# Optimization experiments

Measured on AMD Instinct MI355X. Metric: run time of the kernel, lower is better.

Reference implementation:

```python
import jax, jax.numpy as jnp
import numpy as np

B, N, C = 2, 4096, 256
H = 8          # num heads
D = C // H     # head dim = 32
SR = 2         # spatial reduction ratio
HID = 1024     # mixffn hidden = 4*C
EPS = 1e-5


def layernorm(x, g, b):
    mu = jnp.mean(x, axis=-1, keepdims=True)
    var = jnp.mean(jnp.square(x - mu), axis=-1, keepdims=True)
    return (x - mu) * jax.lax.rsqrt(var + EPS) * g + b


def conv2d(x, w, b, stride, pad, groups=1):
    out = jax.lax.conv_general_dilated(
        x, w, (stride, stride), [(pad, pad), (pad, pad)],
        dimension_numbers=("NCHW", "OIHW", "NCHW"), feature_group_count=groups)
    return out + b[None, :, None, None]


def setup_inputs() -> dict:
    key = jax.random.key(0)
    ks = jax.random.split(key, 20)
    s = lambda k, shape, scale=0.02: jax.random.normal(k, shape, jnp.float32) * scale
    return {
        "x": jax.random.normal(ks[0], (B, N, C), jnp.float32),
        "h": 64, "w": 64,
        "ln1_g": jnp.ones((C,), jnp.float32), "ln1_b": jnp.zeros((C,), jnp.float32),
        "q_w": s(ks[1], (C, C)),
        "kv_w": s(ks[2], (2 * C, C)),
        "sr_w": s(ks[3], (C, C, SR, SR)), "sr_b": jnp.zeros((C,), jnp.float32),
        "srn_g": jnp.ones((C,), jnp.float32), "srn_b": jnp.zeros((C,), jnp.float32),
        "proj_w": s(ks[4], (C, C)), "proj_b": jnp.zeros((C,), jnp.float32),
        "ln2_g": jnp.ones((C,), jnp.float32), "ln2_b": jnp.zeros((C,), jnp.float32),
        "fc1_w": s(ks[5], (HID, C)), "fc1_b": jnp.zeros((HID,), jnp.float32),
        "pe_w": s(ks[6], (HID, 1, 3, 3)), "pe_b": jnp.zeros((HID,), jnp.float32),
        "fc2_w": s(ks[7], (C, HID)), "fc2_b": jnp.zeros((C,), jnp.float32),
    }


def reference(x, h, w, ln1_g, ln1_b, q_w, kv_w, sr_w, sr_b, srn_g, srn_b,
              proj_w, proj_b, ln2_g, ln2_b, fc1_w, fc1_b, pe_w, pe_b, fc2_w, fc2_b):
    b_, n_, c_ = x.shape
    # ---- attention branch ----
    xn = layernorm(x, ln1_g, ln1_b)
    q = jnp.einsum("bnc,oc->bno", xn, q_w).reshape(b_, n_, H, D).transpose(0, 2, 1, 3)  # [B,H,N,D]
    # spatial-reduction of KV
    x_kv = xn.reshape(b_, h, w, c_).transpose(0, 3, 1, 2)              # [B,C,h,w]
    x_kv = conv2d(x_kv, sr_w, sr_b, stride=SR, pad=0)                  # [B,C,h/SR,w/SR]
    nkv = (h // SR) * (w // SR)
    x_kv = x_kv.reshape(b_, c_, nkv).transpose(0, 2, 1)                # [B,Nkv,C]
    x_kv = layernorm(x_kv, srn_g, srn_b)
    kv = jnp.einsum("bnc,oc->bno", x_kv, kv_w).reshape(b_, nkv, 2, H, D)
    k = kv[:, :, 0].transpose(0, 2, 1, 3)                              # [B,H,Nkv,D]
    v = kv[:, :, 1].transpose(0, 2, 1, 3)
    scale = D ** -0.5
    att = jax.nn.softmax(jnp.einsum("bhxd,bhyd->bhxy", q, k) * scale, axis=-1)
    o = jnp.einsum("bhxy,bhyd->bhxd", att, v)                          # [B,H,N,D]
    o = o.transpose(0, 2, 1, 3).reshape(b_, n_, c_)
    o = jnp.einsum("bnc,oc->bno", o, proj_w) + proj_b
    x = x + o
    # ---- Mix-FFN branch ----
    xn2 = layernorm(x, ln2_g, ln2_b)
    xf = xn2.reshape(b_, h, w, c_).transpose(0, 3, 1, 2)               # [B,C,h,w]
    xf = jnp.einsum("bchw,oc->bohw", xf, fc1_w) + fc1_b[None, :, None, None]
    xf = conv2d(xf, pe_w, pe_b, stride=1, pad=1, groups=HID)           # depthwise 3x3
    xf = jax.nn.gelu(xf, approximate=False)
    xf = jnp.einsum("bchw,oc->bohw", xf, fc2_w) + fc2_b[None, :, None, None]
    xf = xf.transpose(0, 2, 3, 1).reshape(b_, n_, c_)
    return x + xf
```

## Files before the change

### kernel.cpp

```cpp
#include <hip/hip_runtime.h>
#include <math.h>

constexpr int BB   = 2;
constexpr int NN   = 4096;
constexpr int CCH  = 256;
constexpr int NH   = 8;
constexpr int HD   = 32;
constexpr int GW   = 64;
constexpr int NKV  = 1024;
constexpr int HIDN = 1024;
constexpr float EPSF = 1e-5f;

typedef short  bf16x8 __attribute__((ext_vector_type(8)));
typedef short  bf16x4 __attribute__((ext_vector_type(4)));
typedef float  f32x4  __attribute__((ext_vector_type(4)));

__device__ __forceinline__ short f2bf(float f) {
    unsigned int u = __float_as_uint(f);
    unsigned int r = (u + 0x7FFFu + ((u >> 16) & 1u)) >> 16;
    return (short)r;
}
__device__ __forceinline__ float bf2f(short s) {
    return __uint_as_float(((unsigned int)(unsigned short)s) << 16);
}
__device__ __forceinline__ void gl16(const void* g, void* l) {
    __builtin_amdgcn_global_load_lds(
        (const __attribute__((address_space(1))) void*)g,
        (__attribute__((address_space(3))) void*)l, 16, 0, 0);
}

__global__ __launch_bounds__(256) void prep_kernel(const float* __restrict__ q_w,
                                                   const float* __restrict__ kv_w,
                                                   const float* __restrict__ proj_w,
                                                   const float* __restrict__ fc1_w,
                                                   const float* __restrict__ fc2_w,
                                                   const float* __restrict__ sr_w,
                                                   short* qwb, short* kvwb, short* pjwb,
                                                   short* f1wb, short* f2wb, short* srwb,
                                                   const float* __restrict__ x,
                                                   const float* __restrict__ ln1_g,
                                                   const float* __restrict__ ln1_b,
                                                   short* __restrict__ xn) {
    __shared__ float pa[4], pb[4];
    int t = threadIdx.x;
    if (blockIdx.x < 4096) {
        int i = blockIdx.x * 256 + t;
        if (i < 65536) { qwb[i] = f2bf(q_w[i] * 0.17677669529663687f); return; }
        i -= 65536;
        if (i < 131072) { kvwb[i] = f2bf(kv_w[i]); return; }
        i -= 131072;
        if (i < 65536) { pjwb[i] = f2bf(proj_w[i]); return; }
        i -= 65536;
        if (i < 262144) { f1wb[i] = f2bf(fc1_w[i]); return; }
        i -= 262144;
        if (i < 262144) { f2wb[i] = f2bf(fc2_w[i]); return; }
        i -= 262144;
        {
            int o = i >> 10, rem = i & 1023, c = rem >> 2, q = rem & 3;
            srwb[o * 1024 + q * 256 + c] = f2bf(sr_w[i]);
        }
        return;
    }
    int row = blockIdx.x - 4096;
    float v = x[row * CCH + t];
    float a = v, b = v * v;
#pragma unroll
    for (int off = 32; off > 0; off >>= 1) {
        a += __shfl_xor(a, off);
        b += __shfl_xor(b, off);
    }
    int w = t >> 6;
    if ((t & 63) == 0) { pa[w] = a; pb[w] = b; }
    __syncthreads();
    a = pa[0] + pa[1] + pa[2] + pa[3];
    b = pb[0] + pb[1] + pb[2] + pb[3];
    float mu = a * (1.0f / CCH);
    float var = b * (1.0f / CCH) - mu * mu;
    float rs = rsqrtf(var + EPSF);
    xn[row * CCH + t] = f2bf((v - mu) * rs * ln1_g[t] + ln1_b[t]);
}

template <bool INBF>
__global__ __launch_bounds__(256) void ln_wave(const void* __restrict__ in,
                                               const float* __restrict__ g,
                                               const float* __restrict__ bta,
                                               short* __restrict__ out) {
    int t = threadIdx.x;
    int w = t >> 6, lane = t & 63;
    int row = blockIdx.x * 4 + w;
    float v[4];
    if (INBF) {
        bf16x4 bv = *(const bf16x4*)&((const short*)in)[(size_t)row * CCH + lane * 4];
#pragma unroll
        for (int j = 0; j < 4; j++) v[j] = bf2f(bv[j]);
    } else {
        float4 fv = *(const float4*)&((const float*)in)[(size_t)row * CCH + lane * 4];
        v[0] = fv.x; v[1] = fv.y; v[2] = fv.z; v[3] = fv.w;
    }
    float a = v[0] + v[1] + v[2] + v[3];
    float b = v[0]*v[0] + v[1]*v[1] + v[2]*v[2] + v[3]*v[3];
#pragma unroll
    for (int off = 1; off < 64; off <<= 1) {
        a += __shfl_xor(a, off);
        b += __shfl_xor(b, off);
    }
    float mu = a * (1.0f / CCH);
    float var = b * (1.0f / CCH) - mu * mu;
    float rs = rsqrtf(var + EPSF);
    bf16x4 ov;
#pragma unroll
    for (int j = 0; j < 4; j++)
        ov[j] = f2bf((v[j] - mu) * rs * g[lane * 4 + j] + bta[lane * 4 + j]);
    *(bf16x4*)&out[(size_t)row * CCH + lane * 4] = ov;
}

template <bool OUTB, int RESMODE>
__device__ __forceinline__ void gemm64_body(const short* __restrict__ A,
                                            const short* __restrict__ W,
                                            const float* __restrict__ bias,
                                            const void* __restrict__ res,
                                            void* __restrict__ outp,
                                            int M, int O, int K, int bx, int by,
                                            short (*As0)[64], short (*Ws0)[64],
                                            short (*As1)[64], short (*Ws1)[64]) {
    int t = threadIdx.x;
    int m0 = by * 64, o0 = bx * 64;
    int w = t >> 6, lane = t & 63;
    int wm = (w >> 1) * 32, wn = (w & 1) * 32;
    int fr = lane & 15, fq = lane >> 4;
    int srow = lane >> 3;
    int sg   = (lane & 7) ^ srow;
    f32x4 acc[2][2];
#pragma unroll
    for (int mi = 0; mi < 2; mi++)
#pragma unroll
        for (int ni = 0; ni < 2; ni++)
            acc[mi][ni] = f32x4{0.f, 0.f, 0.f, 0.f};

    auto stage = [&](short (*Asb)[64], short (*Wsb)[64], int k0) {
#pragma unroll
        for (int r = 0; r < 2; r++) {
            int rowA = r * 32 + w * 8 + srow;
            gl16(&A[(size_t)(m0 + rowA) * K + k0 + sg * 8], &Asb[r * 32 + w * 8][0]);
            gl16(&W[(size_t)(o0 + rowA) * K + k0 + sg * 8], &Wsb[r * 32 + w * 8][0]);
        }
    };
    auto compute = [&](short (*Asb)[64], short (*Wsb)[64]) {
#pragma unroll
        for (int half = 0; half < 2; half++) {
            bf16x8 af[2], wf[2];
#pragma unroll
            for (int mi = 0; mi < 2; mi++) {
                int row = wm + mi * 16 + fr;
                af[mi] = *(const bf16x8*)&Asb[row][(((half << 2) | fq) ^ (row & 7)) * 8];
            }
#pragma unroll
            for (int ni = 0; ni < 2; ni++) {
                int row = wn + ni * 16 + fr;
                wf[ni] = *(const bf16x8*)&Wsb[row][(((half << 2) | fq) ^ (row & 7)) * 8];
            }
#pragma unroll
            for (int mi = 0; mi < 2; mi++)
#pragma unroll
                for (int ni = 0; ni < 2; ni++)
                    acc[mi][ni] = __builtin_amdgcn_mfma_f32_16x16x32_bf16(
                        af[mi], wf[ni], acc[mi][ni], 0, 0, 0);
        }
    };

    stage(As0, Ws0, 0);
    __syncthreads();
    for (int k0 = 0; k0 < K; k0 += 128) {
        if (k0 + 64 < K) stage(As1, Ws1, k0 + 64);
        compute(As0, Ws0);
        __syncthreads();
        if (k0 + 128 < K) stage(As0, Ws0, k0 + 128);
        if (k0 + 64 < K) compute(As1, Ws1);
        __syncthreads();
    }
#pragma unroll
    for (int mi = 0; mi < 2; mi++)
#pragma unroll
        for (int ni = 0; ni < 2; ni++)
#pragma unroll
            for (int r = 0; r < 4; r++) {
                int m = m0 + wm + mi * 16 + fq * 4 + r;
                int o = o0 + wn + ni * 16 + fr;
                float v = acc[mi][ni][r];
                if (bias) v += bias[o];
                if (RESMODE == 1) v += ((const float*)res)[(size_t)m * O + o];
                if (RESMODE == 2) v += bf2f(((const short*)res)[(size_t)m * O + o]);
                if (OUTB) ((short*)outp)[(size_t)m * O + o] = f2bf(v);
                else      ((float*)outp)[(size_t)m * O + o] = v;
            }
}

template <bool OUTB, int RESMODE>
__global__ __launch_bounds__(256, 4) void gemm64(const short* __restrict__ A,
                                                 const short* __restrict__ W,
                                                 const float* __restrict__ bias,
                                                 const void* __restrict__ res,
                                                 void* __restrict__ outp,
                                                 int M, int O, int K) {
    __shared__ short As0[64][64], Ws0[64][64];
    __shared__ short As1[64][64], Ws1[64][64];
    gemm64_body<OUTB, RESMODE>(A, W, bias, res, outp, M, O, K,
                               blockIdx.x, blockIdx.y, As0, Ws0, As1, Ws1);
}

__device__ __forceinline__ void sr_body(const short* __restrict__ xn,
                                        const short* __restrict__ Wsr,
                                        const float* __restrict__ sr_b,
                                        float* __restrict__ srtmp, int bx, int by,
                                        short (*As0)[64], short (*As1)[64],
                                        short (*Ws0)[64], short (*Ws1)[64]) {
    int t = threadIdx.x;
    int m0 = by * 32, o0 = bx * 64;
    int w = t >> 6, lane = t & 63;
    int wm = (w >> 1) * 16, wn = (w & 1) * 32;
    int fr = lane & 15, fq = lane >> 4;
    int srow = lane >> 3;
    int sg   = (lane & 7) ^ srow;
    int arow = w * 8 + srow;
    int p = m0 + arow;
    int b = p >> 10, pp = p & 1023, ii = pp >> 5, jj = pp & 31;
    int nbase = ii * 128 + jj * 2;
    size_t xbase = (size_t)(b * NN) * CCH;
    f32x4 acc[2];
    acc[0] = f32x4{0.f, 0.f, 0.f, 0.f};
    acc[1] = f32x4{0.f, 0.f, 0.f, 0.f};

    auto stage = [&](short (*Asb)[64], short (*Wsb)[64], int k0) {
        int q = k0 >> 8, c0 = k0 & 255;
        int n = nbase + (q >> 1) * 64 + (q & 1);
        gl16(&xn[xbase + (size_t)n * CCH + c0 + sg * 8], &Asb[w * 8][0]);
#pragma unroll
        for (int r = 0; r < 2; r++)
            gl16(&Wsr[(size_t)(o0 + r * 32 + w * 8 + srow) * 1024 + k0 + sg * 8],
                 &Wsb[r * 32 + w * 8][0]);
    };
    auto compute = [&](short (*Asb)[64], short (*Wsb)[64]) {
#pragma unroll
        for (int half = 0; half < 2; half++) {
            int cg = (half << 2) | fq;
            int rowa = wm + fr;
            bf16x8 af = *(const bf16x8*)&Asb[rowa][(cg ^ (rowa & 7)) * 8];
            bf16x8 wf[2];
#pragma unroll
            for (int ni = 0; ni < 2; ni++) {
                int row = wn + ni * 16 + fr;
                wf[ni] = *(const bf16x8*)&Wsb[row][(cg ^ (row & 7)) * 8];
            }
#pragma unroll
            for (int ni = 0; ni < 2; ni++)
                acc[ni] = __builtin_amdgcn_mfma_f32_16x16x32_bf16(
                    af, wf[ni], acc[ni], 0, 0, 0);
        }
    };

    stage(As0, Ws0, 0);
    __syncthreads();
    for (int k0 = 0; k0 < 1024; k0 += 128) {
        if (k0 + 64 < 1024) stage(As1, Ws1, k0 + 64);
        compute(As0, Ws0);
        __syncthreads();
        if (k0 + 128 < 1024) stage(As0, Ws0, k0 + 128);
        compute(As1, Ws1);
        __syncthreads();
    }
#pragma unroll
    for (int ni = 0; ni < 2; ni++)
#pragma unroll
        for (int r = 0; r < 4; r++) {
            int m = m0 + wm + fq * 4 + r;
            int o = o0 + wn + ni * 16 + fr;
            srtmp[(size_t)m * CCH + o] = acc[ni][r] + sr_b[o];
        }
}

__global__ __launch_bounds__(256, 4) void qsr_gemm(const short* __restrict__ xn,
                                                   const short* __restrict__ qwb,
                                                   short* __restrict__ qb,
                                                   const short* __restrict__ srwb,
                                                   const float* __restrict__ sr_b,
                                                   float* __restrict__ srtmp) {
    __shared__ short pool[16384];
    int i = blockIdx.x;
    if (i < 512) {
        gemm64_body<true, 0>(xn, qwb, nullptr, nullptr, qb, BB * NN, CCH, CCH,
                             i & 3, i >> 2,
                             (short(*)[64])(pool),
                             (short(*)[64])(pool + 4096),
                             (short(*)[64])(pool + 8192),
                             (short(*)[64])(pool + 12288));
    } else {
        i -= 512;
        sr_body(xn, srwb, sr_b, srtmp, i & 3, i >> 2,
                (short(*)[64])(pool),
                (short(*)[64])(pool + 2048),
                (short(*)[64])(pool + 4096),
                (short(*)[64])(pool + 8192));
    }
}

__global__ __launch_bounds__(256, 2) void gemm_fc1(const short* __restrict__ A,
                                                   const short* __restrict__ W,
                                                   const float* __restrict__ bias,
                                                   short* __restrict__ outp,
                                                   int M, int O, int K) {
    __shared__ short As0[128][64], Ws0[128][64];
    __shared__ short As1[128][64], Ws1[128][64];
    int t = threadIdx.x;
    int m0 = blockIdx.y * 128, o0 = blockIdx.x * 128;
    int w = t >> 6, lane = t & 63;
    int wm = (w >> 1) * 64, wn = (w & 1) * 64;
    int fr = lane & 15, fq = lane >> 4;
    int srow = lane >> 3;
    int sg   = (lane & 7) ^ srow;
    f32x4 acc[4][4];
#pragma unroll
    for (int mi = 0; mi < 4; mi++)
#pragma unroll
        for (int ni = 0; ni < 4; ni++)
            acc[mi][ni] = f32x4{0.f, 0.f, 0.f, 0.f};

    auto stage = [&](short (*Asb)[64], short (*Wsb)[64], int k0) {
#pragma unroll
        for (int r = 0; r < 4; r++) {
            int rowA = r * 32 + w * 8 + srow;
            gl16(&A[(size_t)(m0 + rowA) * K + k0 + sg * 8], &Asb[r * 32 + w * 8][0]);
            gl16(&W[(size_t)(o0 + rowA) * K + k0 + sg * 8], &Wsb[r * 32 + w * 8][0]);
        }
    };
    auto compute = [&](short (*Asb)[64], short (*Wsb)[64]) {
#pragma unroll
        for (int half = 0; half < 2; half++) {
            bf16x8 af[4], wf[4];
#pragma unroll
            for (int mi = 0; mi < 4; mi++) {
                int row = wm + mi * 16 + fr;
                af[mi] = *(const bf16x8*)&Asb[row][(((half << 2) | fq) ^ (row & 7)) * 8];
            }
#pragma unroll
            for (int ni = 0; ni < 4; ni++) {
                int row = wn + ni * 16 + fr;
                wf[ni] = *(const bf16x8*)&Wsb[row][(((half << 2) | fq) ^ (row & 7)) * 8];
            }
#pragma unroll
            for (int mi = 0; mi < 4; mi++)
#pragma unroll
                for (int ni = 0; ni < 4; ni++)
                    acc[mi][ni] = __builtin_amdgcn_mfma_f32_16x16x32_bf16(
                        af[mi], wf[ni], acc[mi][ni], 0, 0, 0);
        }
    };

    stage(As0, Ws0, 0);
    __syncthreads();
    for (int k0 = 0; k0 < K; k0 += 128) {
        if (k0 + 64 < K) stage(As1, Ws1, k0 + 64);
        compute(As0, Ws0);
        __syncthreads();
        if (k0 + 128 < K) stage(As0, Ws0, k0 + 128);
        if (k0 + 64 < K) compute(As1, Ws1);
        __syncthreads();
    }
#pragma unroll
    for (int mi = 0; mi < 4; mi++)
#pragma unroll
        for (int ni = 0; ni < 4; ni++)
#pragma unroll
            for (int r = 0; r < 4; r++) {
                int m = m0 + wm + mi * 16 + fq * 4 + r;
                int o = o0 + wn + ni * 16 + fr;
                outp[(size_t)m * O + o] = f2bf(acc[mi][ni][r] + bias[o]);
            }
}

__global__ __launch_bounds__(256, 4) void kv_gemm(const short* __restrict__ A,
                                                  const short* __restrict__ W,
                                                  short* __restrict__ kvk,
                                                  short* __restrict__ vt) {
    __shared__ short As0[64][64], Ws0[64][64];
    __shared__ short As1[64][64], Ws1[64][64];
    int t = threadIdx.x;
    int m0 = blockIdx.y * 64, o0 = blockIdx.x * 64;
    int w = t >> 6, lane = t & 63;
    int wm = (w >> 1) * 32, wn = (w & 1) * 32;
    int fr = lane & 15, fq = lane >> 4;
    int srow = lane >> 3;
    int sg   = (lane & 7) ^ srow;
    f32x4 acc[2][2];
#pragma unroll
    for (int mi = 0; mi < 2; mi++)
#pragma unroll
        for (int ni = 0; ni < 2; ni++)
            acc[mi][ni] = f32x4{0.f, 0.f, 0.f, 0.f};

    auto stage = [&](short (*Asb)[64], short (*Wsb)[64], int k0) {
#pragma unroll
        for (int r = 0; r < 2; r++) {
            int rowA = r * 32 + w * 8 + srow;
            gl16(&A[(size_t)(m0 + rowA) * CCH + k0 + sg * 8], &Asb[r * 32 + w * 8][0]);
            gl16(&W[(size_t)(o0 + rowA) * CCH + k0 + sg * 8], &Wsb[r * 32 + w * 8][0]);
        }
    };
    auto compute = [&](short (*Asb)[64], short (*Wsb)[64]) {
#pragma unroll
        for (int half = 0; half < 2; half++) {
            bf16x8 af[2], wf[2];
#pragma unroll
            for (int mi = 0; mi < 2; mi++) {
                int row = wm + mi * 16 + fr;
                af[mi] = *(const bf16x8*)&Asb[row][(((half << 2) | fq) ^ (row & 7)) * 8];
            }
#pragma unroll
            for (int ni = 0; ni < 2; ni++) {
                int row = wn + ni * 16 + fr;
                wf[ni] = *(const bf16x8*)&Wsb[row][(((half << 2) | fq) ^ (row & 7)) * 8];
            }
#pragma unroll
            for (int mi = 0; mi < 2; mi++)
#pragma unroll
                for (int ni = 0; ni < 2; ni++)
                    acc[mi][ni] = __builtin_amdgcn_mfma_f32_16x16x32_bf16(
                        af[mi], wf[ni], acc[mi][ni], 0, 0, 0);
        }
    };

    stage(As0, Ws0, 0);
    __syncthreads();
    stage(As1, Ws1, 64);
    compute(As0, Ws0);
    __syncthreads();
    stage(As0, Ws0, 128);
    compute(As1, Ws1);
    __syncthreads();
    stage(As1, Ws1, 192);
    compute(As0, Ws0);
    __syncthreads();
    compute(As1, Ws1);

#pragma unroll
    for (int mi = 0; mi < 2; mi++)
#pragma unroll
        for (int ni = 0; ni < 2; ni++) {
            int o = o0 + wn + ni * 16 + fr;
            int mbase = m0 + wm + mi * 16 + fq * 4;
            if (o < 256) {
#pragma unroll
                for (int r = 0; r < 4; r++)
                    kvk[(size_t)(mbase + r) * 256 + o] = f2bf(acc[mi][ni][r]);
            } else {
                int h = (o - 256) >> 5, d = (o - 256) & 31;
                int b = mbase >> 10, y0 = mbase & 1023;
                bf16x4 pv;
#pragma unroll
                for (int r = 0; r < 4; r++) pv[r] = f2bf(acc[mi][ni][r]);
                *(bf16x4*)&vt[((size_t)((b * NH + h) * HD) + d) * NKV + y0] = pv;
            }
        }
}

__global__ __launch_bounds__(256, 3) void attn_mfma(const short* __restrict__ qb,
                                                    const short* __restrict__ kvk,
                                                    const short* __restrict__ vt,
                                                    short* __restrict__ o) {
    int blk = blockIdx.x;
    int qt = blk & 31; int hh = (blk >> 5) & 7; int b = blk >> 8;
    int t = threadIdx.x; int w = t >> 6; int lane = t & 63;
    int fr = lane & 15, fq = lane >> 4;
    __shared__ short Ks0[128][32], Ks1[128][32];
    __shared__ short Vt0[64][64],  Vt1[64][64];
    __shared__ short Ps[4][2][16][64];
    int n0 = qt * 128 + w * 16;
    bf16x8 qa[2];
#pragma unroll
    for (int mi = 0; mi < 2; mi++)
        qa[mi] = *(const bf16x8*)&qb[((size_t)(b * NN) + n0 + mi * 64 + fr) * CCH + hh * HD + fq * 8];
    f32x4 oacc[2][2];
    float lst[2][4];
#pragma unroll
    for (int mi = 0; mi < 2; mi++) {
#pragma unroll
        for (int nd = 0; nd < 2; nd++) oacc[mi][nd] = f32x4{0.f, 0.f, 0.f, 0.f};
#pragma unroll
        for (int r = 0; r < 4; r++) lst[mi][r] = 0.f;
    }

    int srowK = lane >> 2;
    int sgK   = (lane & 3) ^ (srowK & 3);
    int srowV = lane >> 3;
    int sgV   = (lane & 7) ^ srowV;

    auto stageKV = [&](short (*Ksb)[32], short (*Vtb)[64], int y0) {
#pragma unroll
        for (int r2 = 0; r2 < 2; r2++) {
            int rowK = r2 * 64 + w * 16 + srowK;
            gl16(&kvk[((size_t)(b * NKV) + y0 + rowK) * 256 + hh * HD + sgK * 8],
                 &Ksb[r2 * 64 + w * 16][0]);
        }
#pragma unroll
        for (int r3 = 0; r3 < 2; r3++) {
            int d = w * 8 + srowV;
            gl16(&vt[((size_t)((b * NH + hh) * HD) + d) * NKV + y0 + r3 * 64 + sgV * 8],
                 &Vtb[r3 * 32 + w * 8][0]);
        }
    };
    auto tile = [&](short (*Ksb)[32], short (*Vtb)[64]) {
#pragma unroll
        for (int h2 = 0; h2 < 2; h2++) {
#pragma unroll
            for (int mi = 0; mi < 2; mi++) {
                f32x4 s[4];
#pragma unroll
                for (int ni = 0; ni < 4; ni++) {
                    int rowk = h2 * 64 + ni * 16 + fr;
                    bf16x8 kb = *(const bf16x8*)&Ksb[rowk][(fq ^ (fr & 3)) * 8];
                    s[ni] = __builtin_amdgcn_mfma_f32_16x16x32_bf16(
                        qa[mi], kb, f32x4{0.f, 0.f, 0.f, 0.f}, 0, 0, 0);
                }
#pragma unroll
                for (int r = 0; r < 4; r++) {
                    int row = fq * 4 + r;
                    float psum = 0.f;
#pragma unroll
                    for (int i = 0; i < 4; i++) {
                        float p = __expf(fminf(s[i][r], 30.f));
                        psum += p;
                        int col = i * 16 + fr;
                        int sgp = ((col >> 3) ^ row) & 7;
                        Ps[w][mi][row][sgp * 8 + (col & 7)] = f2bf(p);
                    }
                    lst[mi][r] += psum;
                }
#pragma unroll
                for (int ks = 0; ks < 2; ks++) {
                    int gk = ks * 4 + fq;
                    bf16x8 pa = *(const bf16x8*)&Ps[w][mi][fr][((gk ^ fr) & 7) * 8];
#pragma unroll
                    for (int nd = 0; nd < 2; nd++) {
                        int rowv = nd * 16 + fr;
                        bf16x8 vb = *(const bf16x8*)&Vtb[h2 * 32 + rowv][((gk ^ (rowv & 7)) & 7) * 8];
                        oacc[mi][nd] = __builtin_amdgcn_mfma_f32_16x16x32_bf16(
                            pa, vb, oacc[mi][nd], 0, 0, 0);
                    }
                }
            }
        }
    };

    stageKV(Ks0, Vt0, 0);
    __syncthreads();
    for (int y0 = 0; y0 < NKV; y0 += 256) {
        if (y0 + 128 < NKV) stageKV(Ks1, Vt1, y0 + 128);
        tile(Ks0, Vt0);
        __syncthreads();
        if (y0 + 256 < NKV) stageKV(Ks0, Vt0, y0 + 256);
        tile(Ks1, Vt1);
        __syncthreads();
    }
#pragma unroll
    for (int mi = 0; mi < 2; mi++)
#pragma unroll
        for (int r = 0; r < 4; r++) {
            float ls = lst[mi][r];
#pragma unroll
            for (int off = 1; off < 16; off <<= 1)
                ls += __shfl_xor(ls, off);
            float inv = 1.f / ls;
            int row = n0 + mi * 64 + fq * 4 + r;
#pragma unroll
            for (int nd = 0; nd < 2; nd++)
                o[((size_t)(b * NN) + row) * CCH + hh * HD + nd * 16 + fr] =
                    f2bf(oacc[mi][nd][r] * inv);
        }
}

__global__ __launch_bounds__(256, 2) void dwconv_gelu(const short* __restrict__ xf,
                                                      const float* __restrict__ pe_w,
                                                      const float* __restrict__ pe_b,
                                                      short* __restrict__ out) {
    int blk = blockIdx.x;
    int cg = blk & 15, sp = (blk >> 4) & 15, b = blk >> 8;
    int r0 = (sp >> 2) * 16, c0 = (sp & 3) * 16;
    int ch0 = cg * 64;
    int t = threadIdx.x;
    __shared__ short tile[18][18][64];
    for (int idx = t; idx < 18 * 18 * 8; idx += 256) {
        int pix = idx >> 3, part = idx & 7;
        int row = pix / 18, col = pix - row * 18;
        int gr = r0 + row - 1, gc = c0 + col - 1;
        bf16x8 v = {0, 0, 0, 0, 0, 0, 0, 0};
        if (gr >= 0 && gr < 64 && gc >= 0 && gc < 64)
            v = *(const bf16x8*)&xf[((size_t)(b * NN) + gr * GW + gc) * HIDN + ch0 + part * 8];
        *(bf16x8*)&tile[row][col][part * 8] = v;
    }
    __syncthreads();
    int cl = t & 63, sg = t >> 6;
    int ch = ch0 + cl;
    float wv[9];
#pragma unroll
    for (int k = 0; k < 9; k++) wv[k] = pe_w[ch * 9 + k];
    float bias = pe_b[ch];
#pragma unroll
    for (int q = 0; q < 4; q++) {
        int lr = sg * 4 + q;
        float cA[3], cB[3], cC[3];
#pragma unroll
        for (int ki = 0; ki < 3; ki++) {
            cA[ki] = bf2f(tile[lr + ki][0][cl]);
            cB[ki] = bf2f(tile[lr + ki][1][cl]);
        }
        for (int cc = 0; cc < 16; cc++) {
#pragma unroll
            for (int ki = 0; ki < 3; ki++) cC[ki] = bf2f(tile[lr + ki][cc + 2][cl]);
            float acc = bias;
#pragma unroll
            for (int ki = 0; ki < 3; ki++)
                acc += cA[ki] * wv[ki * 3] + cB[ki] * wv[ki * 3 + 1] + cC[ki] * wv[ki * 3 + 2];
            float z = 0.7978845608f * (acc + 0.044715f * acc * acc * acc);
            float e = __expf(-2.f * fabsf(z));
            float th = (1.f - e) / (1.f + e);
            th = (z < 0.f) ? -th : th;
            float gg = 0.5f * acc * (1.f + th);
            out[((size_t)(b * NN) + (r0 + lr) * GW + c0 + cc) * HIDN + ch] = f2bf(gg);
#pragma unroll
            for (int ki = 0; ki < 3; ki++) { cA[ki] = cB[ki]; cB[ki] = cC[ki]; }
        }
    }
}

extern "C" void kernel_launch(void* const* d_in, const int* in_sizes, int n_in,
                              void* d_out, int out_size, void* d_ws, size_t ws_size,
                              hipStream_t stream) {
    const float* x      = (const float*)d_in[0];
    const float* ln1_g  = (const float*)d_in[3];
    const float* ln1_b  = (const float*)d_in[4];
    const float* q_w    = (const float*)d_in[5];
    const float* kv_w   = (const float*)d_in[6];
    const float* sr_w   = (const float*)d_in[7];
    const float* sr_b   = (const float*)d_in[8];
    const float* srn_g  = (const float*)d_in[9];
    const float* srn_b  = (const float*)d_in[10];
    const float* proj_w = (const float*)d_in[11];
    const float* proj_b = (const float*)d_in[12];
    const float* ln2_g  = (const float*)d_in[13];
    const float* ln2_b  = (const float*)d_in[14];
    const float* fc1_w  = (const float*)d_in[15];
    const float* fc1_b  = (const float*)d_in[16];
    const float* pe_w   = (const float*)d_in[17];
    const float* pe_b   = (const float*)d_in[18];
    const float* fc2_w  = (const float*)d_in[19];
    const float* fc2_b  = (const float*)d_in[20];
    float* out = (float*)d_out;

    char* base = (char*)d_ws;
    short* xn    = (short*)(base);
    short* qb    = (short*)(base + (4ull  << 20));
    float* srtmp = (float*)(base + (12ull << 20));
    short* xkvn  = (short*)(base + (14ull << 20));
    short* kvk   = (short*)(base + (15ull << 20));
    short* vtb   = (short*)(base + (17ull << 20));
    short* obf   = (short*)(base + (18ull << 20));
    short* x1    = (short*)(base + (22ull << 20));
    short* xf1   = (short*)(base + (30ull << 20));
    short* xf2g  = (short*)(base + (46ull << 20));
    short* qwb   = (short*)(base + (62ull << 20));
    short* kvwb  = qwb  + 65536;
    short* pjwb  = kvwb + 131072;
    short* f1wb  = pjwb + 65536;
    short* f2wb  = f1wb + 262144;
    short* srwb  = f2wb + 262144;

    prep_kernel<<<4096 + BB * NN, 256, 0, stream>>>(q_w, kv_w, proj_w, fc1_w, fc2_w, sr_w,
                                                    qwb, kvwb, pjwb, f1wb, f2wb, srwb,
                                                    x, ln1_g, ln1_b, xn);
    qsr_gemm<<<768, 256, 0, stream>>>(xn, qwb, qb, srwb, sr_b, srtmp);
    ln_wave<false><<<BB * NKV / 4, 256, 0, stream>>>(srtmp, srn_g, srn_b, xkvn);
    {
        dim3 g(512 / 64, (BB * NKV) / 64);
        kv_gemm<<<g, 256, 0, stream>>>(xkvn, kvwb, kvk, vtb);
    }
    attn_mfma<<<BB * NH * (NN / 128), 256, 0, stream>>>(qb, kvk, vtb, obf);
    {
        dim3 g(CCH / 64, (BB * NN) / 64);
        gemm64<true, 1><<<g, 256, 0, stream>>>(obf, pjwb, proj_b, x, x1, BB * NN, CCH, CCH);
    }
    ln_wave<true><<<BB * NN / 4, 256, 0, stream>>>(x1, ln2_g, ln2_b, xn);
    {
        dim3 g(HIDN / 128, (BB * NN) / 128);
        gemm_fc1<<<g, 256, 0, stream>>>(xn, f1wb, fc1_b, xf1, BB * NN, HIDN, CCH);
    }
    dwconv_gelu<<<BB * 256, 256, 0, stream>>>(xf1, pe_w, pe_b, xf2g);
    {
        dim3 g(CCH / 64, (BB * NN) / 64);
        gemm64<false, 2><<<g, 256, 0, stream>>>(xf2g, f2wb, fc2_b, x1, out, BB * NN, CCH, HIDN);
    }
}
```

Baseline: 116.7 us.

## Permute key order in V^T and P to pack bf16 conversion and vector LDS stores

The KV projection epilogue now writes V^T with key indices permuted inside each 64-key block. This lets the attention kernel give each lane four contiguous P columns, convert them with v_cvt_pk_bf16_f32 and store them as a single 8-byte LDS write instead of four scalar 2-byte stores. It also adds s_setprio around the MFMA sections to favour matrix issue across waves. The cost is that the V^T writes become scattered scalar stores in the projection epilogue.

After: 115.6 us, median of 2. Within noise of the previous version (-0.9%).

```diff
diff --git a/kernel.cpp b/kernel.cpp
--- a/kernel.cpp
+++ b/kernel.cpp
@@ -22,6 +22,11 @@
 }
 __device__ __forceinline__ float bf2f(short s) {
     return __uint_as_float(((unsigned int)(unsigned short)s) << 16);
+}
+__device__ __forceinline__ unsigned int cvtpk_bf16(float a, float b) {
+    unsigned int r;
+    asm("v_cvt_pk_bf16_f32 %0, %1, %2" : "=v"(r) : "v"(a), "v"(b));
+    return r;
 }
 __device__ __forceinline__ void gl16(const void* g, void* l) {
     __builtin_amdgcn_global_load_lds(
@@ -454,10 +459,14 @@
             } else {
                 int h = (o - 256) >> 5, d = (o - 256) & 31;
                 int b = mbase >> 10, y0 = mbase & 1023;
-                bf16x4 pv;
-#pragma unroll
-                for (int r = 0; r < 4; r++) pv[r] = f2bf(acc[mi][ni][r]);
-                *(bf16x4*)&vt[((size_t)((b * NH + h) * HD) + d) * NKV + y0] = pv;
+                size_t rowbase = ((size_t)((b * NH + h) * HD) + d) * NKV + (y0 >> 6) * 64;
+                int y4 = y0 & 63;
+#pragma unroll
+                for (int r = 0; r < 4; r++) {
+                    int y64 = y4 + r;
+                    int s = (y64 & 15) * 4 + (y64 >> 4);
+                    vt[rowbase + s] = f2bf(acc[mi][ni][r]);
+                }
             }
         }
 }
@@ -513,6 +522,7 @@
 #pragma unroll
             for (int mi = 0; mi < 2; mi++) {
                 f32x4 s[4];
+                __builtin_amdgcn_s_setprio(1);
 #pragma unroll
                 for (int ni = 0; ni < 4; ni++) {
                     int rowk = h2 * 64 + ni * 16 + fr;
@@ -520,32 +530,34 @@
                     s[ni] = __builtin_amdgcn_mfma_f32_16x16x32_bf16(
                         qa[mi], kb, f32x4{0.f, 0.f, 0.f, 0.f}, 0, 0, 0);
                 }
+                __builtin_amdgcn_s_setprio(0);
 #pragma unroll
                 for (int r = 0; r < 4; r++) {
                     int row = fq * 4 + r;
-                    float psum = 0.f;
-#pragma unroll
-                    for (int i = 0; i < 4; i++) {
-                        float p = __expf(fminf(s[i][r], 30.f));
-                        psum += p;
-                        int col = i * 16 + fr;
-                        int sgp = ((col >> 3) ^ row) & 7;
-                        Ps[w][mi][row][sgp * 8 + (col & 7)] = f2bf(p);
-                    }
-                    lst[mi][r] += psum;
+                    float p0 = __expf(fminf(s[0][r], 30.f));
+                    float p1 = __expf(fminf(s[1][r], 30.f));
+                    float p2 = __expf(fminf(s[2][r], 30.f));
+                    float p3 = __expf(fminf(s[3][r], 30.f));
+                    lst[mi][r] += (p0 + p1) + (p2 + p3);
+                    unsigned int w0 = cvtpk_bf16(p0, p1);
+                    unsigned int w1 = cvtpk_bf16(p2, p3);
+                    int gp = (fr >> 1) ^ (row & 7);
+                    *(uint2*)&Ps[w][mi][row][gp * 8 + (fr & 1) * 4] = make_uint2(w0, w1);
                 }
+                __builtin_amdgcn_s_setprio(1);
 #pragma unroll
                 for (int ks = 0; ks < 2; ks++) {
                     int gk = ks * 4 + fq;
-                    bf16x8 pa = *(const bf16x8*)&Ps[w][mi][fr][((gk ^ fr) & 7) * 8];
+                    bf16x8 pa = *(const bf16x8*)&Ps[w][mi][fr][(gk ^ (fr & 7)) * 8];
 #pragma unroll
                     for (int nd = 0; nd < 2; nd++) {
                         int rowv = nd * 16 + fr;
-                        bf16x8 vb = *(const bf16x8*)&Vtb[h2 * 32 + rowv][((gk ^ (rowv & 7)) & 7) * 8];
+                        bf16x8 vb = *(const bf16x8*)&Vtb[h2 * 32 + rowv][(gk ^ (rowv & 7)) * 8];
                         oacc[mi][nd] = __builtin_amdgcn_mfma_f32_16x16x32_bf16(
                             pa, vb, oacc[mi][nd], 0, 0, 0);
                     }
                 }
+                __builtin_amdgcn_s_setprio(0);
             }
         }
     };
```
